# Optimization experiments

Hardware: AMD Instinct MI355X
Metric: run time of the kernel (lower is better)

The kernel has to match this reference:

```python
import jax, jax.numpy as jnp
import numpy as np
from jax import lax

TIME_LENGTH = 256.0  # init kwarg time_length


def setup_inputs() -> dict:
    key = jax.random.key(0)
    ks = jax.random.split(key, 8)
    seq_len, batch, in_sz, hid = 256, 256, 1024, 1024
    w_std = 0.03  # ~ xavier_normal for fan (1025, 1024)
    x = jax.random.normal(ks[0], (seq_len, batch, in_sz), dtype=jnp.float32)
    def w(k):
        return jax.random.normal(k, (in_sz + 1, hid), dtype=jnp.float32) * w_std
    return {
        "x": x,
        "W_ii_0": w(ks[1]), "W_if_0": w(ks[2]), "W_ig_0": w(ks[3]),
        "b_i_0": jnp.zeros((hid,), jnp.float32),
        "b_f_0": jnp.zeros((hid,), jnp.float32),
        "b_g_0": jnp.zeros((hid,), jnp.float32),
        "W_ii_1": w(ks[4]), "W_if_1": w(ks[5]), "W_ig_1": w(ks[6]),
        "b_i_1": jnp.zeros((hid,), jnp.float32),
        "b_f_1": jnp.zeros((hid,), jnp.float32),
        "b_g_1": jnp.zeros((hid,), jnp.float32),
    }


def _cell(inp, c, t, W_i, W_f, W_g, b_i, b_f, b_g):
    # inp: [B, D]; append normalized time column -> [B, D+1]
    tc = jnp.full((inp.shape[0], 1), t / TIME_LENGTH, dtype=inp.dtype)
    xt = jnp.concatenate([inp, tc], axis=1)
    i_t = jax.nn.sigmoid(xt @ W_i + b_i)
    f_t = jax.nn.sigmoid(xt @ W_f + b_f)
    g_t = jax.nn.sigmoid(xt @ W_g + b_g)
    return f_t * c + i_t * g_t


def reference(x, W_ii_0, W_if_0, W_ig_0, b_i_0, b_f_0, b_g_0,
              W_ii_1, W_if_1, W_ig_1, b_i_1, b_f_1, b_g_1):
    seq_len, batch, _ = x.shape
    hid = W_ii_0.shape[1]
    c_init = jnp.zeros((2, batch, hid), dtype=x.dtype)

    def step(c, xt_t):
        x_t, t = xt_t
        c0 = _cell(x_t, c[0], t, W_ii_0, W_if_0, W_ig_0, b_i_0, b_f_0, b_g_0)
        c1 = _cell(c0, c[1], t, W_ii_1, W_if_1, W_ig_1, b_i_1, b_f_1, b_g_1)
        return jnp.stack([c0, c1]), None

    ts = jnp.arange(seq_len, dtype=x.dtype)
    c_n, _ = lax.scan(step, c_init, (x, ts))
    return c_n  # [num_layers=2, batch, hidden]
```

## Files before the change

kernel.cpp:

```cpp
#include <hip/hip_runtime.h>
#include <hip/hip_bf16.h>

#define SEQ   256
#define BATCH 256
#define HID   1024
#define KDIM  1024
#define MTOT  (SEQ*BATCH)
#define BH    (BATCH*HID)

typedef __bf16 bf16x8 __attribute__((ext_vector_type(8)));
typedef float  f32x4  __attribute__((ext_vector_type(4)));

__device__ __forceinline__ ushort f2b(float f){
    __hip_bfloat16 h = __float2bfloat16(f);
    return __builtin_bit_cast(ushort, h);
}
__device__ __forceinline__ float b2f(ushort u){
    __hip_bfloat16 h = __builtin_bit_cast(__hip_bfloat16, u);
    return __bfloat162float(h);
}

__global__ void cvt_x(const float4* __restrict__ x, ushort4* __restrict__ o){
    int i = blockIdx.x * blockDim.x + threadIdx.x;
    float4 v = x[i];
    ushort4 r;
    r.x = f2b(v.x); r.y = f2b(v.y); r.z = f2b(v.z); r.w = f2b(v.w);
    o[i] = r;
}

__global__ void cvt_w(const float* __restrict__ W, ushort* __restrict__ Wt){
    __shared__ float tile[32][33];
    int tx = threadIdx.x & 31, ty = threadIdx.x >> 5;
    int kb = blockIdx.x * 32, nb = blockIdx.y * 32;
    #pragma unroll
    for (int j = 0; j < 32; j += 8)
        tile[ty + j][tx] = W[(size_t)(kb + ty + j) * HID + nb + tx];
    __syncthreads();
    #pragma unroll
    for (int j = 0; j < 32; j += 8)
        Wt[(size_t)(nb + ty + j) * KDIM + kb + tx] = f2b(tile[tx][ty + j]);
}

__global__ void cvt_time(const float* __restrict__ W, float* __restrict__ wt){
    int i = blockIdx.x * blockDim.x + threadIdx.x;
    wt[i] = W[(size_t)KDIM * HID + i];
}

__global__ __launch_bounds__(256) void gemm_gate(
        const ushort* __restrict__ A, const ushort* __restrict__ Wt,
        const float* __restrict__ wtime, const float* __restrict__ bias,
        ushort* __restrict__ G)
{
    __shared__ ushort As[128 * 32];
    __shared__ ushort Bs[128 * 32];

    const int tid  = threadIdx.x;
    const int lane = tid & 63;
    const int wid  = tid >> 6;
    const int wrow = wid >> 1;
    const int wcol = wid & 1;
    const size_t m0 = (size_t)blockIdx.x * 128;
    const int    n0 = blockIdx.y * 128;

    f32x4 acc[4][4];
    #pragma unroll
    for (int i = 0; i < 4; ++i)
        #pragma unroll
        for (int j = 0; j < 4; ++j)
            acc[i][j] = (f32x4){0.f, 0.f, 0.f, 0.f};

    const int lr = lane & 15;
    const int lg = lane >> 4;
    const int srow   = lane >> 2;
    const int schunk = lane & 3;

    for (int k0 = 0; k0 < KDIM; k0 += 32){
        #pragma unroll
        for (int c = 0; c < 2; ++c){
            const int r = wid * 32 + c * 16;
            const ushort* gA = A  + (m0 + r + srow) * KDIM + k0 + schunk * 8;
            __builtin_amdgcn_global_load_lds(
                (const __attribute__((address_space(1))) void*)gA,
                (__attribute__((address_space(3))) void*)(As + r * 32), 16, 0, 0);
            const ushort* gB = Wt + ((size_t)(n0 + r + srow)) * KDIM + k0 + schunk * 8;
            __builtin_amdgcn_global_load_lds(
                (const __attribute__((address_space(1))) void*)gB,
                (__attribute__((address_space(3))) void*)(Bs + r * 32), 16, 0, 0);
        }
        __syncthreads();

        bf16x8 a[4], b[4];
        #pragma unroll
        for (int m = 0; m < 4; ++m)
            a[m] = *(const bf16x8*)&As[(wrow * 64 + m * 16 + lr) * 32 + lg * 8];
        #pragma unroll
        for (int n = 0; n < 4; ++n)
            b[n] = *(const bf16x8*)&Bs[(wcol * 64 + n * 16 + lr) * 32 + lg * 8];

        #pragma unroll
        for (int m = 0; m < 4; ++m)
            #pragma unroll
            for (int n = 0; n < 4; ++n)
                acc[m][n] = __builtin_amdgcn_mfma_f32_16x16x32_bf16(a[m], b[n], acc[m][n], 0, 0, 0);
        __syncthreads();
    }

    #pragma unroll
    for (int m = 0; m < 4; ++m){
        #pragma unroll
        for (int n = 0; n < 4; ++n){
            const int gcol = n0 + wcol * 64 + n * 16 + lr;
            const float wt_c = wtime[gcol];
            const float bi_c = bias[gcol];
            #pragma unroll
            for (int r = 0; r < 4; ++r){
                const size_t grow = m0 + wrow * 64 + m * 16 + lg * 4 + r;
                const int t = (int)(grow >> 8);
                const float pre = acc[m][n][r] + (float)t * (1.0f / 256.0f) * wt_c + bi_c;
                const float s = 1.0f / (1.0f + __expf(-pre));
                G[grow * HID + gcol] = f2b(s);
            }
        }
    }
}

__global__ void scan0(const ushort* __restrict__ gi, const ushort* __restrict__ gf,
                      const ushort* __restrict__ gg, ushort* __restrict__ c0b,
                      float* __restrict__ out){
    int idx = blockIdx.x * blockDim.x + threadIdx.x;
    float c = 0.f;
    for (int t = 0; t < SEQ; ++t){
        size_t off = (size_t)t * BH + idx;
        float i = b2f(gi[off]);
        float f = b2f(gf[off]);
        float g = b2f(gg[off]);
        c = f * c + i * g;
        c0b[off] = f2b(c);
    }
    out[idx] = c;
}

__global__ void scan1(const ushort* __restrict__ gi, const ushort* __restrict__ gf,
                      const ushort* __restrict__ gg, float* __restrict__ out){
    int idx = blockIdx.x * blockDim.x + threadIdx.x;
    float c = 0.f;
    for (int t = 0; t < SEQ; ++t){
        size_t off = (size_t)t * BH + idx;
        float i = b2f(gi[off]);
        float f = b2f(gf[off]);
        float g = b2f(gg[off]);
        c = f * c + i * g;
    }
    out[BH + idx] = c;
}

extern "C" void kernel_launch(void* const* d_in, const int* in_sizes, int n_in,
                              void* d_out, int out_size, void* d_ws, size_t ws_size,
                              hipStream_t stream){
    const float* x  = (const float*)d_in[0];
    const float* W0[3] = {(const float*)d_in[1], (const float*)d_in[2], (const float*)d_in[3]};
    const float* b0[3] = {(const float*)d_in[4], (const float*)d_in[5], (const float*)d_in[6]};
    const float* W1[3] = {(const float*)d_in[7], (const float*)d_in[8], (const float*)d_in[9]};
    const float* b1[3] = {(const float*)d_in[10], (const float*)d_in[11], (const float*)d_in[12]};
    float* out = (float*)d_out;

    char* ws = (char*)d_ws;
    ushort* xb  = (ushort*)ws;
    ushort* gi  = (ushort*)(ws + (size_t)134217728);
    ushort* gf  = (ushort*)(ws + (size_t)268435456);
    ushort* gg  = (ushort*)(ws + (size_t)402653184);
    ushort* Wt  = (ushort*)(ws + (size_t)536870912);
    float*  wtm = (float*)(ws + (size_t)536870912 + (size_t)6 * 2097152);
    ushort* gates[3] = {gi, gf, gg};

    cvt_x<<<MTOT * KDIM / 4 / 256, 256, 0, stream>>>((const float4*)x, (ushort4*)xb);

    dim3 tgrid(32, 32);
    for (int j = 0; j < 3; ++j){
        cvt_w  <<<tgrid, 256, 0, stream>>>(W0[j], Wt + (size_t)j * 1048576);
        cvt_time<<<4, 256, 0, stream>>>(W0[j], wtm + j * 1024);
        cvt_w  <<<tgrid, 256, 0, stream>>>(W1[j], Wt + (size_t)(3 + j) * 1048576);
        cvt_time<<<4, 256, 0, stream>>>(W1[j], wtm + (3 + j) * 1024);
    }

    dim3 ggrid(MTOT / 128, HID / 128);

    for (int j = 0; j < 3; ++j)
        gemm_gate<<<ggrid, 256, 0, stream>>>(xb, Wt + (size_t)j * 1048576,
                                             wtm + j * 1024, b0[j], gates[j]);
    scan0<<<BH / 256, 256, 0, stream>>>(gi, gf, gg, xb, out);

    for (int j = 0; j < 3; ++j)
        gemm_gate<<<ggrid, 256, 0, stream>>>(xb, Wt + (size_t)(3 + j) * 1048576,
                                             wtm + (3 + j) * 1024, b1[j], gates[j]);
    scan1<<<BH / 256, 256, 0, stream>>>(gi, gf, gg, out);
}
```

Before: 2.132 ms.

## Fuse three gate GEMMs into one N=3072 GEMM with double buffering and XCD-aware tiling

Concatenates the three gate weight matrices so each layer runs one GEMM with N=3072 that writes an interleaved gate buffer. The GEMM gains double-buffered LDS staging, an XOR swizzle against LDS bank conflicts, and a block-index remap that groups tiles sharing the same A rows onto one XCD for L2 reuse. The scans read the interleaved layout. The aim is fewer launches, more reuse of A across gates, and load latency overlapped with MFMA, at the cost of twice the LDS and strided gate reads in the scans.

Result: faster. 1.767 ms (-17.1%).

```diff
diff --git a/kernel.cpp b/kernel.cpp
--- a/kernel.cpp
+++ b/kernel.cpp
@@ -7,6 +7,7 @@
 #define KDIM  1024
 #define MTOT  (SEQ*BATCH)
 #define BH    (BATCH*HID)
+#define NF    3072
 
 typedef __bf16 bf16x8 __attribute__((ext_vector_type(8)));
 typedef float  f32x4  __attribute__((ext_vector_type(4)));
@@ -41,26 +42,36 @@
         Wt[(size_t)(nb + ty + j) * KDIM + kb + tx] = f2b(tile[tx][ty + j]);
 }
 
-__global__ void cvt_time(const float* __restrict__ W, float* __restrict__ wt){
+__global__ void prep_cols(const float* __restrict__ W, const float* __restrict__ b,
+                          float* __restrict__ wtv, float* __restrict__ bcat){
     int i = blockIdx.x * blockDim.x + threadIdx.x;
-    wt[i] = W[(size_t)KDIM * HID + i];
-}
-
-__global__ __launch_bounds__(256) void gemm_gate(
+    wtv[i]  = W[(size_t)KDIM * HID + i];
+    bcat[i] = b[i];
+}
+
+__global__ __launch_bounds__(256) void gemm_gate3(
         const ushort* __restrict__ A, const ushort* __restrict__ Wt,
-        const float* __restrict__ wtime, const float* __restrict__ bias,
+        const float* __restrict__ wtv, const float* __restrict__ bcat,
         ushort* __restrict__ G)
 {
-    __shared__ ushort As[128 * 32];
-    __shared__ ushort Bs[128 * 32];
+    __shared__ ushort As[2][128 * 32];
+    __shared__ ushort Bs[2][128 * 32];
 
     const int tid  = threadIdx.x;
     const int lane = tid & 63;
     const int wid  = tid >> 6;
     const int wrow = wid >> 1;
     const int wcol = wid & 1;
-    const size_t m0 = (size_t)blockIdx.x * 128;
-    const int    n0 = blockIdx.y * 128;
+
+    const int bid  = blockIdx.x;
+    const int xcd  = bid & 7;
+    const int slot = bid >> 3;
+    const int nh   = slot / 768;
+    const int rem  = slot - nh * 768;
+    const int mp   = rem / 12;
+    const int nb   = rem - mp * 12 + nh * 12;
+    const size_t m0 = ((size_t)(xcd * 64 + mp)) * 128;
+    const int    n0 = nb * 128;
 
     f32x4 acc[4][4];
     #pragma unroll
@@ -73,36 +84,47 @@
     const int lg = lane >> 4;
     const int srow   = lane >> 2;
     const int schunk = lane & 3;
-
-    for (int k0 = 0; k0 < KDIM; k0 += 32){
+    const int sk   = (schunk ^ ((srow >> 1) & 3)) * 8;
+    const int axor = (lg ^ ((lr >> 1) & 3)) * 8;
+
+    int buf = 0;
+    auto stage = [&](int bsel, int k0){
         #pragma unroll
         for (int c = 0; c < 2; ++c){
             const int r = wid * 32 + c * 16;
-            const ushort* gA = A  + (m0 + r + srow) * KDIM + k0 + schunk * 8;
+            const ushort* gA = A + (m0 + r + srow) * KDIM + k0 + sk;
             __builtin_amdgcn_global_load_lds(
                 (const __attribute__((address_space(1))) void*)gA,
-                (__attribute__((address_space(3))) void*)(As + r * 32), 16, 0, 0);
-            const ushort* gB = Wt + ((size_t)(n0 + r + srow)) * KDIM + k0 + schunk * 8;
+                (__attribute__((address_space(3))) void*)(&As[bsel][r * 32]), 16, 0, 0);
+            const ushort* gB = Wt + (size_t)(n0 + r + srow) * KDIM + k0 + sk;
             __builtin_amdgcn_global_load_lds(
                 (const __attribute__((address_space(1))) void*)gB,
-                (__attribute__((address_space(3))) void*)(Bs + r * 32), 16, 0, 0);
+                (__attribute__((address_space(3))) void*)(&Bs[bsel][r * 32]), 16, 0, 0);
         }
-        __syncthreads();
+    };
+
+    stage(0, 0);
+    __syncthreads();
+
+    for (int kt = 0; kt < 32; ++kt){
+        if (kt != 31) stage(buf ^ 1, (kt + 1) * 32);
 
         bf16x8 a[4], b[4];
         #pragma unroll
         for (int m = 0; m < 4; ++m)
-            a[m] = *(const bf16x8*)&As[(wrow * 64 + m * 16 + lr) * 32 + lg * 8];
+            a[m] = *(const bf16x8*)&As[buf][(wrow * 64 + m * 16 + lr) * 32 + axor];
         #pragma unroll
         for (int n = 0; n < 4; ++n)
-            b[n] = *(const bf16x8*)&Bs[(wcol * 64 + n * 16 + lr) * 32 + lg * 8];
+            b[n] = *(const bf16x8*)&Bs[buf][(wcol * 64 + n * 16 + lr) * 32 + axor];
 
         #pragma unroll
         for (int m = 0; m < 4; ++m)
             #pragma unroll
             for (int n = 0; n < 4; ++n)
                 acc[m][n] = __builtin_amdgcn_mfma_f32_16x16x32_bf16(a[m], b[n], acc[m][n], 0, 0, 0);
+
         __syncthreads();
+        buf ^= 1;
     }
 
     #pragma unroll
@@ -110,45 +132,45 @@
         #pragma unroll
         for (int n = 0; n < 4; ++n){
             const int gcol = n0 + wcol * 64 + n * 16 + lr;
-            const float wt_c = wtime[gcol];
-            const float bi_c = bias[gcol];
+            const float wt_c = wtv[gcol];
+            const float bi_c = bcat[gcol];
             #pragma unroll
             for (int r = 0; r < 4; ++r){
                 const size_t grow = m0 + wrow * 64 + m * 16 + lg * 4 + r;
                 const int t = (int)(grow >> 8);
                 const float pre = acc[m][n][r] + (float)t * (1.0f / 256.0f) * wt_c + bi_c;
                 const float s = 1.0f / (1.0f + __expf(-pre));
-                G[grow * HID + gcol] = f2b(s);
+                G[grow * NF + gcol] = f2b(s);
             }
         }
     }
 }
 
-__global__ void scan0(const ushort* __restrict__ gi, const ushort* __restrict__ gf,
-                      const ushort* __restrict__ gg, ushort* __restrict__ c0b,
+__global__ void scan0(const ushort* __restrict__ G, ushort* __restrict__ c0b,
                       float* __restrict__ out){
     int idx = blockIdx.x * blockDim.x + threadIdx.x;
+    int b = idx >> 10, h = idx & 1023;
     float c = 0.f;
     for (int t = 0; t < SEQ; ++t){
-        size_t off = (size_t)t * BH + idx;
-        float i = b2f(gi[off]);
-        float f = b2f(gf[off]);
-        float g = b2f(gg[off]);
+        size_t base = (size_t)(t * BATCH + b) * NF + h;
+        float i = b2f(G[base]);
+        float f = b2f(G[base + 1024]);
+        float g = b2f(G[base + 2048]);
         c = f * c + i * g;
-        c0b[off] = f2b(c);
+        c0b[(size_t)(t * BATCH + b) * KDIM + h] = f2b(c);
     }
     out[idx] = c;
 }
 
-__global__ void scan1(const ushort* __restrict__ gi, const ushort* __restrict__ gf,
-                      const ushort* __restrict__ gg, float* __restrict__ out){
+__global__ void scan1(const ushort* __restrict__ G, float* __restrict__ out){
     int idx = blockIdx.x * blockDim.x + threadIdx.x;
+    int b = idx >> 10, h = idx & 1023;
     float c = 0.f;
     for (int t = 0; t < SEQ; ++t){
-        size_t off = (size_t)t * BH + idx;
-        float i = b2f(gi[off]);
-        float f = b2f(gf[off]);
-        float g = b2f(gg[off]);
+        size_t base = (size_t)(t * BATCH + b) * NF + h;
+        float i = b2f(G[base]);
+        float f = b2f(G[base + 1024]);
+        float g = b2f(G[base + 2048]);
         c = f * c + i * g;
     }
     out[BH + idx] = c;
@@ -166,32 +188,27 @@
 
     char* ws = (char*)d_ws;
     ushort* xb  = (ushort*)ws;
-    ushort* gi  = (ushort*)(ws + (size_t)134217728);
-    ushort* gf  = (ushort*)(ws + (size_t)268435456);
-    ushort* gg  = (ushort*)(ws + (size_t)402653184);
-    ushort* Wt  = (ushort*)(ws + (size_t)536870912);
-    float*  wtm = (float*)(ws + (size_t)536870912 + (size_t)6 * 2097152);
-    ushort* gates[3] = {gi, gf, gg};
+    ushort* G   = (ushort*)(ws + (size_t)134217728);
+    ushort* Wt0 = (ushort*)(ws + (size_t)536870912);
+    ushort* Wt1 = (ushort*)(ws + (size_t)543162368);
+    float*  wtv0 = (float*)(ws + (size_t)549453824);
+    float*  bc0  = (float*)(ws + (size_t)549453824 + 12288);
+    float*  wtv1 = (float*)(ws + (size_t)549453824 + 24576);
+    float*  bc1  = (float*)(ws + (size_t)549453824 + 36864);
 
     cvt_x<<<MTOT * KDIM / 4 / 256, 256, 0, stream>>>((const float4*)x, (ushort4*)xb);
 
     dim3 tgrid(32, 32);
     for (int j = 0; j < 3; ++j){
-        cvt_w  <<<tgrid, 256, 0, stream>>>(W0[j], Wt + (size_t)j * 1048576);
-        cvt_time<<<4, 256, 0, stream>>>(W0[j], wtm + j * 1024);
-        cvt_w  <<<tgrid, 256, 0, stream>>>(W1[j], Wt + (size_t)(3 + j) * 1048576);
-        cvt_time<<<4, 256, 0, stream>>>(W1[j], wtm + (3 + j) * 1024);
-    }
-
-    dim3 ggrid(MTOT / 128, HID / 128);
-
-    for (int j = 0; j < 3; ++j)
-        gemm_gate<<<ggrid, 256, 0, stream>>>(xb, Wt + (size_t)j * 1048576,
-                                             wtm + j * 1024, b0[j], gates[j]);
-    scan0<<<BH / 256, 256, 0, stream>>>(gi, gf, gg, xb, out);
-
-    for (int j = 0; j < 3; ++j)
-        gemm_gate<<<ggrid, 256, 0, stream>>>(xb, Wt + (size_t)(3 + j) * 1048576,
-                                             wtm + (3 + j) * 1024, b1[j], gates[j]);
-    scan1<<<BH / 256, 256, 0, stream>>>(gi, gf, gg, out);
-}
+        cvt_w<<<tgrid, 256, 0, stream>>>(W0[j], Wt0 + (size_t)j * 1048576);
+        cvt_w<<<tgrid, 256, 0, stream>>>(W1[j], Wt1 + (size_t)j * 1048576);
+        prep_cols<<<4, 256, 0, stream>>>(W0[j], b0[j], wtv0 + j * 1024, bc0 + j * 1024);
+        prep_cols<<<4, 256, 0, stream>>>(W1[j], b1[j], wtv1 + j * 1024, bc1 + j * 1024);
+    }
+
+    gemm_gate3<<<12288, 256, 0, stream>>>(xb, Wt0, wtv0, bc0, G);
+    scan0<<<BH / 256, 256, 0, stream>>>(G, xb, out);
+
+    gemm_gate3<<<12288, 256, 0, stream>>>(xb, Wt1, wtv1, bc1, G);
+    scan1<<<BH / 256, 256, 0, stream>>>(G, out);
+}
```
